# Kernel optimization log

Measured on AMD Instinct MI355X. Metric: run time of the kernel, lower is better.

## Reference

```python
import jax, jax.numpy as jnp
import numpy as np

N = 50000
E = 800000
IN_FEAT = 256
HIDDEN = 256
NUM_CLASS = 10
NUM_GRAPHS = 512
LAYERS = 2


def setup_inputs() -> dict:
    key = jax.random.key(0)
    ks = jax.random.split(key, 10)
    x = jax.random.normal(ks[0], (N, IN_FEAT), dtype=jnp.float32)
    edge_index = jax.random.randint(ks[1], (2, E), 0, N, dtype=jnp.int32)
    batch = jnp.sort(jax.random.randint(ks[2], (N,), 0, NUM_GRAPHS, dtype=jnp.int32))
    s_in = 1.0 / np.sqrt(IN_FEAT)
    s_h = 1.0 / np.sqrt(HIDDEN)
    enc_W = jax.random.uniform(ks[3], (IN_FEAT, HIDDEN), jnp.float32, -s_in, s_in)
    enc_b = jax.random.uniform(ks[4], (HIDDEN,), jnp.float32, -s_in, s_in)
    conv_W = jax.random.uniform(ks[5], (LAYERS, HIDDEN, HIDDEN), jnp.float32, -s_h, s_h)
    conv_b = jax.random.uniform(ks[6], (LAYERS, HIDDEN), jnp.float32, -s_h, s_h)
    out_W = jax.random.uniform(ks[7], (HIDDEN, NUM_CLASS), jnp.float32, -s_h, s_h)
    out_b = jax.random.uniform(ks[8], (NUM_CLASS,), jnp.float32, -s_h, s_h)
    return {"x": x, "edge_index": edge_index, "batch": batch,
            "enc_W": enc_W, "enc_b": enc_b,
            "conv_W": conv_W, "conv_b": conv_b,
            "out_W": out_W, "out_b": out_b}


def _gcn_conv(x, row, col, deg_norm_edge, W, b):
    # PyG GCNConv: linear transform, then normalized scatter-add aggregation.
    h = x @ W                                   # [N, H]
    msg = h[row] * deg_norm_edge[:, None]       # [E+N, H] gather + scale
    out = jax.ops.segment_sum(msg, col, num_segments=N)  # scatter-add
    return out + b


def reference(x, edge_index, batch, enc_W, enc_b, conv_W, conv_b, out_W, out_b):
    # self-loops appended once (same structure every layer)
    loops = jnp.arange(N, dtype=edge_index.dtype)
    row = jnp.concatenate([edge_index[0], loops])  # source
    col = jnp.concatenate([edge_index[1], loops])  # target
    deg = jax.ops.segment_sum(jnp.ones_like(col, dtype=x.dtype), col, num_segments=N)
    dinv = jnp.where(deg > 0, jax.lax.rsqrt(deg), 0.0)
    norm = dinv[row] * dinv[col]                # symmetric GCN normalization per edge

    h = x @ enc_W + enc_b
    for i in range(LAYERS):
        h = jax.nn.relu(_gcn_conv(h, row, col, norm, conv_W[i], conv_b[i]))

    # global_mean_pool over `batch` segment ids
    sums = jax.ops.segment_sum(h, batch, num_segments=NUM_GRAPHS)
    cnts = jax.ops.segment_sum(jnp.ones((N,), dtype=h.dtype), batch, num_segments=NUM_GRAPHS)
    pooled = sums / jnp.maximum(cnts, 1.0)[:, None]

    # dropout is identity in eval mode
    return pooled @ out_W + out_b
```

## Files before the change

kernel.cpp:

```cpp
#include <hip/hip_runtime.h>

#define NN 50000
#define NE 800000
#define HD 256
#define NG 512
#define NC 10
#define GEMM_G ((NN + 31) / 32)
#define NP 196
#define HB 200
#define CHUNK (NE / HB)
#define NODES_PER_HB (NN / HB)

typedef unsigned short u16;
typedef unsigned char u8;
typedef short v8s __attribute__((ext_vector_type(8)));
typedef float v4f __attribute__((ext_vector_type(4)));
typedef float v2f __attribute__((ext_vector_type(2)));
typedef u16 v4u __attribute__((ext_vector_type(4)));

static __device__ __forceinline__ float bf2f(u16 u) {
    return __uint_as_float(((unsigned)u) << 16);
}
static __device__ __forceinline__ u16 f2bf(float f) {
    unsigned u = __float_as_uint(f);
    unsigned r = (u + 0x7fffu + ((u >> 16) & 1u)) >> 16;
    return (u16)r;
}
static __device__ __forceinline__ int clampi(int v, int lo, int hi) {
    return min(max(v, lo), hi);
}
static __device__ __forceinline__ float ldf(const void* p, size_t i, int isbf) {
    return isbf ? bf2f(((const u16*)p)[i]) : ((const float*)p)[i];
}

static __device__ __forceinline__ u8 f32_to_fp8(float f) {
#if __has_builtin(__builtin_amdgcn_cvt_pk_fp8_f32)
    int r = __builtin_amdgcn_cvt_pk_fp8_f32(f, f, 0, false);
    return (u8)(r & 0xff);
#else
    float a = fabsf(f);
    unsigned s = (__float_as_uint(f) >> 31) << 7;
    if (a < 0.0009765625f) return (u8)s;
    a = fminf(a, 448.f);
    if (a < 0.015625f) {
        int m = (int)(a * 512.f + 0.5f);
        return (u8)(s | min(m, 7));
    }
    unsigned u = __float_as_uint(a);
    unsigned r = u + 0x0007FFFFu + ((u >> 20) & 1u);
    int e = (int)(r >> 23) - 127 + 7;
    if (e > 15) return (u8)(s | 0x7E);
    unsigned m = (r >> 20) & 7u;
    return (u8)(s | ((unsigned)e << 3) | m);
#endif
}
static __device__ __forceinline__ v4f fp8x4_to_f32(unsigned v) {
#if __has_builtin(__builtin_amdgcn_cvt_pk_f32_fp8)
    v2f lo = __builtin_amdgcn_cvt_pk_f32_fp8(v, false);
    v2f hi = __builtin_amdgcn_cvt_pk_f32_fp8(v, true);
    return (v4f){lo[0], lo[1], hi[0], hi[1]};
#else
    v4f o;
#pragma unroll
    for (int j = 0; j < 4; j++) {
        unsigned b = (v >> (8 * j)) & 0xffu;
        unsigned e = (b >> 3) & 15u, m = b & 7u;
        float val = e ? __uint_as_float(((e + 120u) << 23) | (m << 20))
                      : (float)m * 0.001953125f;
        o[j] = (b & 0x80u) ? -val : val;
    }
    return o;
#endif
}

__global__ void k_detect(const u16* __restrict__ xu, int* __restrict__ mode) {
    __shared__ int cnt;
    if (threadIdx.x == 0) cnt = 0;
    __syncthreads();
    int bad = 0;
    for (int i = threadIdx.x; i < 4096; i += 256) {
        float v = bf2f(xu[2 * i]);
        float av = fabsf(v);
        if (av > 100.f || (av < 1e-3f && av != 0.f)) bad++;
    }
    atomicAdd(&cnt, bad);
    __syncthreads();
    if (threadIdx.x == 0) mode[0] = (cnt > 1024) ? 0 : 1;
}

__global__ void k_prep(const void* __restrict__ enc_W, const void* __restrict__ conv_W,
                       const void* __restrict__ enc_b, const void* __restrict__ conv_b,
                       const void* __restrict__ out_b,
                       u16* __restrict__ Wp, float* __restrict__ biasf,
                       const int* __restrict__ modep) {
    int md = modep[0];
    int b = blockIdx.x;
    if (b < 768) {
        int wi = b >> 8;
        int n = b & 255, k = threadIdx.x;
        const void* W = (wi == 0) ? enc_W : conv_W;
        size_t off = (wi == 0) ? 0 : (size_t)(wi - 1) * HD * HD;
        int nt = n >> 4, m = n & 15;
        int ks = k >> 5, q = (k >> 3) & 3, j = k & 7;
        size_t idx = ((((size_t)nt * 8 + ks) * 64) + q * 16 + m) * 8 + j;
        Wp[(size_t)wi * HD * HD + idx] = f2bf(ldf(W, off + (size_t)k * HD + n, md));
    } else {
        for (int j = threadIdx.x; j < 768 + NC; j += 256) {
            float v = (j < 256) ? ldf(enc_b, j, md)
                    : (j < 768) ? ldf(conv_b, j - 256, md)
                                : ldf(out_b, j - 768, md);
            biasf[j] = v;
        }
    }
}

static __device__ __forceinline__ void hist_body(
        int b, const int* __restrict__ ecol, const int* __restrict__ batch,
        int* __restrict__ bh, int* __restrict__ gptr, int* hist) {
    int tid = threadIdx.x;
    if (tid < NP) hist[tid] = 0;
    __syncthreads();
    int e0 = b * CHUNK;
    for (int i = tid; i < CHUNK; i += 256) {
        int c = clampi(ecol[e0 + i], 0, NN - 1);
        atomicAdd(&hist[c >> 8], 1);
    }
    int n0 = b * NODES_PER_HB;
    for (int i = tid; i < NODES_PER_HB; i += 256) {
        int idx = n0 + i;
        int bb = clampi(batch[idx], 0, NG - 1);
        int bp = (idx == 0) ? -1 : clampi(batch[idx - 1], 0, NG - 1);
        for (int g = bp + 1; g <= bb; g++) gptr[g] = idx;
        if (idx == NN - 1)
            for (int g = bb + 1; g <= NG; g++) gptr[g] = NN;
    }
    __syncthreads();
    if (tid < NP) bh[(size_t)tid * HB + b] = hist[tid];
}

static __device__ __forceinline__ void scat_body(
        int b, const int* __restrict__ erow, const int* __restrict__ ecol,
        const int* __restrict__ pptr, const int* __restrict__ base,
        unsigned* __restrict__ pairbuf, int* lfill) {
    int tid = threadIdx.x;
    if (tid < NP) lfill[tid] = 0;
    __syncthreads();
    int e0 = b * CHUNK;
    for (int i = tid; i < CHUNK; i += 256) {
        int c = clampi(ecol[e0 + i], 0, NN - 1);
        int rw = clampi(erow[e0 + i], 0, NN - 1);
        int p = c >> 8;
        int r = atomicAdd(&lfill[p], 1);
        int pos = pptr[p] + base[(size_t)p * HB + b] + r;
        pairbuf[pos] = ((unsigned)rw << 8) | (unsigned)(c & 255);
    }
}

static __device__ __forceinline__ void gemm_body(
        int bid, u16* As, const void* __restrict__ A, const u16* __restrict__ Wp,
        const float* __restrict__ biasf, void* __restrict__ out,
        int M, int hasBias, int outFp8, int amode) {
    int tid = threadIdx.x;
    int wave = tid >> 6;
    int lane = tid & 63;
    int row0 = bid * 32;
    if (row0 >= M) return;
    int m = lane & 15, q = lane >> 4;

#pragma unroll
    for (int it = 0; it < 4; it++) {
        int fb = it * 4 + wave;
        int mt = fb >> 3, ks = fb & 7;
        int row = min(row0 + mt * 16 + m, M - 1);
        int colE = ks * 32 + q * 8;
        v8s v;
        if (amode) {
            v = *(const v8s*)((const u16*)A + (size_t)row * HD + colE);
        } else {
            const float* af = (const float*)A + (size_t)row * HD + colE;
            v4f x0 = *(const v4f*)af;
            v4f x1 = *(const v4f*)(af + 4);
            v[0] = (short)f2bf(x0[0]); v[1] = (short)f2bf(x0[1]);
            v[2] = (short)f2bf(x0[2]); v[3] = (short)f2bf(x0[3]);
            v[4] = (short)f2bf(x1[0]); v[5] = (short)f2bf(x1[1]);
            v[6] = (short)f2bf(x1[2]); v[7] = (short)f2bf(x1[3]);
        }
        *(v8s*)&As[((size_t)fb * 64 + lane) * 8] = v;
    }
    __syncthreads();

    v4f acc[2][4];
#pragma unroll
    for (int i = 0; i < 2; i++)
#pragma unroll
        for (int j = 0; j < 4; j++) acc[i][j] = (v4f){0.f, 0.f, 0.f, 0.f};

    const u16* wp = Wp + (size_t)wave * 4 * 8 * 64 * 8;

#pragma unroll
    for (int ks = 0; ks < 8; ks++) {
        v8s bfr[4];
#pragma unroll
        for (int nt = 0; nt < 4; nt++)
            bfr[nt] = *(const v8s*)(wp + ((size_t)(nt * 8 + ks) * 64 + lane) * 8);
        v8s a[2];
#pragma unroll
        for (int mt = 0; mt < 2; mt++)
            a[mt] = *(const v8s*)&As[((size_t)(mt * 8 + ks) * 64 + lane) * 8];
#pragma unroll
        for (int mt = 0; mt < 2; mt++)
#pragma unroll
            for (int nt = 0; nt < 4; nt++)
                acc[mt][nt] = __builtin_amdgcn_mfma_f32_16x16x32_bf16(
                    a[mt], bfr[nt], acc[mt][nt], 0, 0, 0);
    }
    if (outFp8) {
#pragma unroll
        for (int mt = 0; mt < 2; mt++) {
#pragma unroll
            for (int nt = 0; nt < 4; nt++) {
                int ocol = wave * 64 + nt * 16 + m;
#pragma unroll
                for (int r = 0; r < 4; r++) {
                    int orow = row0 + mt * 16 + q * 4 + r;
                    if (orow < M)
                        ((u8*)out)[(size_t)orow * HD + ocol] =
                            f32_to_fp8(acc[mt][nt][r] * 32.f);
                }
            }
        }
    } else {
#pragma unroll
        for (int mt = 0; mt < 2; mt++) {
#pragma unroll
            for (int nt = 0; nt < 4; nt++) {
                int ocol = wave * 64 + nt * 16 + m;
                float badd = hasBias ? biasf[ocol] : 0.f;
#pragma unroll
                for (int r = 0; r < 4; r++) {
                    int orow = row0 + mt * 16 + q * 4 + r;
                    if (orow < M)
                        ((u16*)out)[(size_t)orow * HD + ocol] =
                            f2bf(acc[mt][nt][r] + badd);
                }
            }
        }
    }
}

__global__ __launch_bounds__(256) void k_gemm(
        const void* __restrict__ A, const u16* __restrict__ Wp,
        const float* __restrict__ biasf, void* __restrict__ out,
        int M, int hasBias, int outFp8,
        const int* __restrict__ modep, int forceBf) {
    __shared__ u16 As[16 * 64 * 8];
    gemm_body(blockIdx.x, As, A, Wp, biasf, out, M, hasBias, outFp8,
              forceBf ? 1 : modep[0]);
}

__global__ __launch_bounds__(256) void k_hist(
        const int* __restrict__ ecol, const int* __restrict__ batch,
        int* __restrict__ bh, int* __restrict__ gptr) {
    __shared__ int hist[NP];
    hist_body(blockIdx.x, ecol, batch, bh, gptr, hist);
}

__global__ __launch_bounds__(256) void k_scat(
        const int* __restrict__ erow, const int* __restrict__ ecol,
        const int* __restrict__ pptr, const int* __restrict__ base,
        unsigned* __restrict__ pairbuf) {
    __shared__ int lfill[NP];
    scat_body(blockIdx.x, erow, ecol, pptr, base, pairbuf, lfill);
}

__global__ __launch_bounds__(256) void k_gemm_hist(
        const void* __restrict__ A, const u16* __restrict__ Wp,
        const float* __restrict__ biasf, void* __restrict__ out,
        int M, int hasBias, const int* __restrict__ modep, int forceBf,
        const int* __restrict__ ecol, const int* __restrict__ batch,
        int* __restrict__ bh, int* __restrict__ gptr) {
    __shared__ u16 As[16 * 64 * 8];
    __shared__ int hist[NP];
    if (blockIdx.x < HB) {
        hist_body(blockIdx.x, ecol, batch, bh, gptr, hist);
    } else {
        gemm_body(blockIdx.x - HB, As, A, Wp, biasf, out, M, hasBias, 0,
                  forceBf ? 1 : modep[0]);
    }
}

__global__ __launch_bounds__(256) void k_scat_gemm1(
        const void* __restrict__ A, const u16* __restrict__ Wp,
        void* __restrict__ out, int M,
        const int* __restrict__ erow, const int* __restrict__ ecol,
        const int* __restrict__ pptr, const int* __restrict__ base,
        unsigned* __restrict__ pairbuf) {
    __shared__ u16 As[16 * 64 * 8];
    __shared__ int lfill[NP];
    if (blockIdx.x < HB) {
        scat_body(blockIdx.x, erow, ecol, pptr, base, pairbuf, lfill);
    } else {
        gemm_body(blockIdx.x - HB, As, A, Wp, nullptr, out, M, 0, 1, 1);
    }
}

__global__ __launch_bounds__(256) void k_scanA(
        const int* __restrict__ bh, int* __restrict__ base, int* __restrict__ ptot) {
    int p = blockIdx.x, t = threadIdx.x;
    int v = (t < HB) ? bh[(size_t)p * HB + t] : 0;
    __shared__ int sh[256];
    sh[t] = v;
    __syncthreads();
    for (int off = 1; off < 256; off <<= 1) {
        int x = (t >= off) ? sh[t - off] : 0;
        __syncthreads();
        sh[t] += x;
        __syncthreads();
    }
    if (t < HB) base[(size_t)p * HB + t] = sh[t] - v;
    if (t == 0) ptot[p] = sh[255];
}

__global__ __launch_bounds__(256) void k_scanB(
        const int* __restrict__ ptot, int* __restrict__ pptr) {
    int t = threadIdx.x;
    int v = (t < NP) ? ptot[t] : 0;
    __shared__ int sh[256];
    sh[t] = v;
    __syncthreads();
    for (int off = 1; off < 256; off <<= 1) {
        int x = (t >= off) ? sh[t - off] : 0;
        __syncthreads();
        sh[t] += x;
        __syncthreads();
    }
    if (t < NP) pptr[t] = sh[t] - v;
    if (t == 0) pptr[NP] = sh[255];
}

__global__ __launch_bounds__(256) void k_part2(
        const int* __restrict__ pptr, const unsigned* __restrict__ pairbuf,
        int* __restrict__ cptr, float* __restrict__ dinv, int* __restrict__ csrc) {
    int p = blockIdx.x, t = threadIdx.x;
    int seg0 = pptr[p], seg1 = pptr[p + 1];
    __shared__ int hist[256], sums[256], fill[256];
    hist[t] = 0;
    fill[t] = 0;
    __syncthreads();
    for (int i = seg0 + t; i < seg1; i += 256)
        atomicAdd(&hist[pairbuf[i] & 255], 1);
    __syncthreads();
    int d = hist[t];
    sums[t] = d;
    __syncthreads();
    for (int off = 1; off < 256; off <<= 1) {
        int x = (t >= off) ? sums[t - off] : 0;
        __syncthreads();
        sums[t] += x;
        __syncthreads();
    }
    int ex = sums[t] - d;
    int c = p * 256 + t;
    if (c < NN) {
        cptr[c] = seg0 + ex;
        dinv[c] = rsqrtf((float)(d + 1));
    }
    if (p == NP - 1 && t == 0) cptr[NN] = NE;
    __syncthreads();
    sums[t] = ex;
    __syncthreads();
    for (int i = seg0 + t; i < seg1; i += 256) {
        unsigned v = pairbuf[i];
        int cl = v & 255;
        int r = atomicAdd(&fill[cl], 1);
        csrc[seg0 + sums[cl] + r] = (int)(v >> 8);
    }
}

__global__ __launch_bounds__(256) void k_aggregate(
        const u8* __restrict__ t, const int* __restrict__ cptr,
        const int* __restrict__ csrc, const float* __restrict__ dinv,
        const float* __restrict__ biasf, u16* __restrict__ out) {
    int wave = threadIdx.x >> 6;
    int lane = threadIdx.x & 63;
    int node = blockIdx.x * 4 + wave;
    if (node >= NN) return;
    int f0 = lane * 4;
    const u8* tf = t + f0;
    float dn = dinv[node];

    unsigned sv = *(const unsigned*)(tf + (size_t)node * HD);
    v4f sd = fp8x4_to_f32(sv);
    float a0 = sd[0] * dn, a1 = sd[1] * dn, a2 = sd[2] * dn, a3 = sd[3] * dn;

    int e0 = cptr[node], e1 = cptr[node + 1];
    e1 = clampi(e1, 0, NE);
    e0 = clampi(e0, 0, e1);
    int e = e0;
    for (; e + 8 <= e1; e += 8) {
        int s[8];
#pragma unroll
        for (int j = 0; j < 8; j++) s[j] = clampi(csrc[e + j], 0, NN - 1);
        unsigned rv[8];
        float wv[8];
#pragma unroll
        for (int j = 0; j < 8; j++) {
            rv[j] = *(const unsigned*)(tf + (size_t)s[j] * HD);
            wv[j] = dinv[s[j]];
        }
#pragma unroll
        for (int j = 0; j < 8; j++) {
            v4f d = fp8x4_to_f32(rv[j]);
            a0 = fmaf(d[0], wv[j], a0); a1 = fmaf(d[1], wv[j], a1);
            a2 = fmaf(d[2], wv[j], a2); a3 = fmaf(d[3], wv[j], a3);
        }
    }
    for (; e < e1; e++) {
        int src = clampi(csrc[e], 0, NN - 1);
        unsigned rv = *(const unsigned*)(tf + (size_t)src * HD);
        float wv = dinv[src];
        v4f d = fp8x4_to_f32(rv);
        a0 = fmaf(d[0], wv, a0); a1 = fmaf(d[1], wv, a1);
        a2 = fmaf(d[2], wv, a2); a3 = fmaf(d[3], wv, a3);
    }
    float sc = dn * 0.03125f;
    v4f b = *(const v4f*)(biasf + f0);
    a0 = fmaxf(a0 * sc + b[0], 0.f);
    a1 = fmaxf(a1 * sc + b[1], 0.f);
    a2 = fmaxf(a2 * sc + b[2], 0.f);
    a3 = fmaxf(a3 * sc + b[3], 0.f);
    v4u o = {f2bf(a0), f2bf(a1), f2bf(a2), f2bf(a3)};
    *(v4u*)(out + (size_t)node * HD + f0) = o;
}

__global__ __launch_bounds__(256) void k_head(
        const u16* __restrict__ h, const int* __restrict__ gptr,
        const void* __restrict__ W, const float* __restrict__ biasf,
        void* __restrict__ outv, const int* __restrict__ modep) {
    int md = modep[0];
    int g = blockIdx.x, f = threadIdx.x;
    int hi = clampi(gptr[g + 1], 0, NN);
    int lo = clampi(gptr[g], 0, hi);
    float s0 = 0.f, s1 = 0.f, s2 = 0.f, s3 = 0.f;
    int i = lo;
    for (; i + 4 <= hi; i += 4) {
        s0 += bf2f(h[(size_t)i * HD + f]);
        s1 += bf2f(h[(size_t)(i + 1) * HD + f]);
        s2 += bf2f(h[(size_t)(i + 2) * HD + f]);
        s3 += bf2f(h[(size_t)(i + 3) * HD + f]);
    }
    for (; i < hi; i++) s0 += bf2f(h[(size_t)i * HD + f]);
    __shared__ float ps[256];
    ps[f] = ((s0 + s1) + (s2 + s3)) / fmaxf((float)(hi - lo), 1.0f);
    __syncthreads();
    if (threadIdx.x < 64) {
        int lane = threadIdx.x;
        float acc[NC];
#pragma unroll
        for (int c = 0; c < NC; c++) acc[c] = 0.f;
        for (int k = lane; k < HD; k += 64) {
            float p = ps[k];
#pragma unroll
            for (int c = 0; c < NC; c++) acc[c] += p * ldf(W, (size_t)k * NC + c, md);
        }
#pragma unroll
        for (int c = 0; c < NC; c++) {
            for (int off = 32; off > 0; off >>= 1)
                acc[c] += __shfl_down(acc[c], off, 64);
        }
        if (lane == 0) {
#pragma unroll
            for (int c = 0; c < NC; c++) {
                float vv = acc[c] + biasf[768 + c];
                if (md) ((u16*)outv)[g * NC + c] = f2bf(vv);
                else    ((float*)outv)[g * NC + c] = vv;
            }
        }
    }
}

extern "C" void kernel_launch(void* const* d_in, const int* in_sizes, int n_in,
                              void* d_out, int out_size, void* d_ws, size_t ws_size,
                              hipStream_t stream) {
    const void* x      = d_in[0];
    const int*  ei     = (const int*)d_in[1];
    const int*  batch  = (const int*)d_in[2];
    const void* enc_W  = d_in[3];
    const void* enc_b  = d_in[4];
    const void* conv_W = d_in[5];
    const void* conv_b = d_in[6];
    const void* out_W  = d_in[7];
    const void* out_b  = d_in[8];

    char* w = (char*)d_ws;
    auto alloc = [&](size_t b) { char* p = w; w += (b + 255) & ~(size_t)255; return p; };
    int*   mode   = (int*)alloc(256);
    float* dinv   = (float*)alloc(NN * 4);
    int*   cptr   = (int*)alloc((NN + 1) * 4);
    int*   gptr   = (int*)alloc((NG + 1) * 4);
    int*   csrc   = (int*)alloc((size_t)NE * 4);
    u16*   Wp     = (u16*)alloc((size_t)3 * HD * HD * 2);
    float* biasf  = (float*)alloc(778 * 4);
    u16*   hbuf   = (u16*)alloc((size_t)NN * HD * 2);
    size_t scratch_need = ((size_t)2 * NP * HB + 2 * NP + 1) * 4 + (size_t)NE * 4 + 1024;
    size_t used = (size_t)(w - (char*)d_ws);
    bool fused = (used + scratch_need <= ws_size);
    char* sb = fused ? alloc(scratch_need) : (char*)hbuf;
    int* bh   = (int*)sb;
    int* base = bh + (size_t)NP * HB;
    int* ptot = base + (size_t)NP * HB;
    int* pptr = ptot + NP;
    unsigned* pairbuf = (unsigned*)(pptr + NP + 1);
    u8* tbuf = (u8*)d_in[0];

    const int* erow = ei;
    const int* ecol = ei + NE;

    k_detect<<<1, 256, 0, stream>>>((const u16*)x, mode);
    k_prep<<<769, 256, 0, stream>>>(enc_W, conv_W, enc_b, conv_b, out_b, Wp, biasf, mode);

    if (fused) {
        k_gemm_hist<<<HB + GEMM_G, 256, 0, stream>>>(
            x, Wp, biasf, hbuf, NN, 1, mode, 0, ecol, batch, bh, gptr);
        k_scanA<<<NP, 256, 0, stream>>>(bh, base, ptot);
        k_scanB<<<1, 256, 0, stream>>>(ptot, pptr);
        k_scat_gemm1<<<HB + GEMM_G, 256, 0, stream>>>(
            hbuf, Wp + (size_t)HD * HD, tbuf, NN, erow, ecol, pptr, base, pairbuf);
        k_part2<<<NP, 256, 0, stream>>>(pptr, pairbuf, cptr, dinv, csrc);
    } else {
        k_hist<<<HB, 256, 0, stream>>>(ecol, batch, bh, gptr);
        k_scanA<<<NP, 256, 0, stream>>>(bh, base, ptot);
        k_scanB<<<1, 256, 0, stream>>>(ptot, pptr);
        k_scat<<<HB, 256, 0, stream>>>(erow, ecol, pptr, base, pairbuf);
        k_part2<<<NP, 256, 0, stream>>>(pptr, pairbuf, cptr, dinv, csrc);
        k_gemm<<<GEMM_G, 256, 0, stream>>>(x, Wp, biasf, hbuf, NN, 1, 0, mode, 0);
        k_gemm<<<GEMM_G, 256, 0, stream>>>(hbuf, Wp + (size_t)HD * HD, nullptr,
                                           tbuf, NN, 0, 1, mode, 1);
    }
    k_aggregate<<<(NN + 3) / 4, 256, 0, stream>>>(tbuf, cptr, csrc, dinv,
                                                  biasf + 256, hbuf);
    k_gemm<<<GEMM_G, 256, 0, stream>>>(hbuf, Wp + (size_t)2 * HD * HD, nullptr,
                                       tbuf, NN, 0, 1, mode, 1);
    k_aggregate<<<(NN + 3) / 4, 256, 0, stream>>>(tbuf, cptr, csrc, dinv,
                                                  biasf + 256 + HD, hbuf);
    k_head<<<NG, 256, 0, stream>>>(hbuf, gptr, out_W, biasf, d_out, mode);
}
```

Baseline: 285.0 us.

## Fuse layer-1 aggregation with layer-2 GEMM and widen aggregate lanes

Adds a fused kernel that gathers and aggregates the layer-1 neighbour messages for 32 nodes into shared memory as bf16, then multiplies the tile by the next conv weight with MFMA and writes fp8 output to a new buffer. This removes one bf16 round trip of the hidden activations and one kernel launch. The aggregation is also rewritten so each lane handles 8 features and the two half-waves split the edges, combined with a cross-half shuffle, giving wider loads and more memory parallelism. The fused path needs an extra N*HD workspace buffer, and the fused kernel runs gather work with fewer waves per node tile, which could lower latency hiding.

```diff
diff --git a/kernel.cpp b/kernel.cpp
--- a/kernel.cpp
+++ b/kernel.cpp
@@ -17,6 +17,7 @@
 typedef float v4f __attribute__((ext_vector_type(4)));
 typedef float v2f __attribute__((ext_vector_type(2)));
 typedef u16 v4u __attribute__((ext_vector_type(4)));
+typedef u16 v8u __attribute__((ext_vector_type(8)));
 
 static __device__ __forceinline__ float bf2f(u16 u) {
     return __uint_as_float(((unsigned)u) << 16);
@@ -248,6 +249,89 @@
     }
 }
 
+static __device__ __forceinline__ void agg_node(
+        const u8* __restrict__ t, const int* __restrict__ cptr,
+        const int* __restrict__ csrc, const float* __restrict__ dinv,
+        const float* __restrict__ biasf, int node, int lane, float* o) {
+    int half = lane >> 5;
+    int f0 = (lane & 31) * 8;
+    const u8* tf = t + f0;
+    float dn = dinv[node];
+    float a[8];
+#pragma unroll
+    for (int k = 0; k < 8; k++) a[k] = 0.f;
+
+    if (half == 0) {
+        uint2 sv = *(const uint2*)(tf + (size_t)node * HD);
+        v4f lo = fp8x4_to_f32(sv.x), hi = fp8x4_to_f32(sv.y);
+#pragma unroll
+        for (int k = 0; k < 4; k++) {
+            a[k] += lo[k] * dn;
+            a[k + 4] += hi[k] * dn;
+        }
+    }
+
+    int e0 = cptr[node], e1 = cptr[node + 1];
+    e1 = clampi(e1, 0, NE);
+    e0 = clampi(e0, 0, e1);
+    int e = e0;
+    for (; e + 16 <= e1; e += 16) {
+        int s[8];
+#pragma unroll
+        for (int j = 0; j < 8; j++)
+            s[j] = clampi(csrc[e + 2 * j + half], 0, NN - 1);
+        uint2 rv[8];
+        float wv[8];
+#pragma unroll
+        for (int j = 0; j < 8; j++) {
+            rv[j] = *(const uint2*)(tf + (size_t)s[j] * HD);
+            wv[j] = dinv[s[j]];
+        }
+#pragma unroll
+        for (int j = 0; j < 8; j++) {
+            v4f lo = fp8x4_to_f32(rv[j].x), hi = fp8x4_to_f32(rv[j].y);
+#pragma unroll
+            for (int k = 0; k < 4; k++) {
+                a[k] = fmaf(lo[k], wv[j], a[k]);
+                a[k + 4] = fmaf(hi[k], wv[j], a[k + 4]);
+            }
+        }
+    }
+    for (; e + 2 <= e1; e += 2) {
+        int s = clampi(csrc[e + half], 0, NN - 1);
+        uint2 rv = *(const uint2*)(tf + (size_t)s * HD);
+        float wv = dinv[s];
+        v4f lo = fp8x4_to_f32(rv.x), hi = fp8x4_to_f32(rv.y);
+#pragma unroll
+        for (int k = 0; k < 4; k++) {
+            a[k] = fmaf(lo[k], wv, a[k]);
+            a[k + 4] = fmaf(hi[k], wv, a[k + 4]);
+        }
+    }
+    if (e < e1 && half == 0) {
+        int s = clampi(csrc[e], 0, NN - 1);
+        uint2 rv = *(const uint2*)(tf + (size_t)s * HD);
+        float wv = dinv[s];
+        v4f lo = fp8x4_to_f32(rv.x), hi = fp8x4_to_f32(rv.y);
+#pragma unroll
+        for (int k = 0; k < 4; k++) {
+            a[k] = fmaf(lo[k], wv, a[k]);
+            a[k + 4] = fmaf(hi[k], wv, a[k + 4]);
+        }
+    }
+#pragma unroll
+    for (int k = 0; k < 8; k++) a[k] += __shfl_xor(a[k], 32, 64);
+
+    float sc = dn * 0.03125f;
+    v4f b0 = *(const v4f*)(biasf + f0);
+    v4f b1 = *(const v4f*)(biasf + f0 + 4);
+#pragma unroll
+    for (int k = 0; k < 4; k++) {
+        o[k] = fmaxf(fmaf(a[k], sc, b0[k]), 0.f);
+        o[k + 4] = fmaxf(fmaf(a[k + 4], sc, b1[k]), 0.f);
+    }
+}
+
 __global__ __launch_bounds__(256) void k_gemm(
         const void* __restrict__ A, const u16* __restrict__ Wp,
         const float* __restrict__ biasf, void* __restrict__ out,
@@ -304,6 +388,89 @@
     }
 }
 
+__global__ __launch_bounds__(256) void k_agg_gemm(
+        const u8* __restrict__ t, const int* __restrict__ cptr,
+        const int* __restrict__ csrc, const float* __restrict__ dinv,
+        const float* __restrict__ biasf, const u16* __restrict__ Wp2,
+        u8* __restrict__ out) {
+    __shared__ u16 As2[32 * 264];
+    int tid = threadIdx.x, wave = tid >> 6, lane = tid & 63;
+    int row0 = blockIdx.x * 32;
+
+    for (int it = 0; it < 8; it++) {
+        int r = wave * 8 + it;
+        int node = row0 + r;
+        float o[8];
+#pragma unroll
+        for (int k = 0; k < 8; k++) o[k] = 0.f;
+        if (node < NN) agg_node(t, cptr, csrc, dinv, biasf, node, lane, o);
+        if (lane < 32) {
+            v8u pk;
+#pragma unroll
+            for (int k = 0; k < 8; k++) pk[k] = f2bf(o[k]);
+            *(v8u*)&As2[r * 264 + lane * 8] = pk;
+        }
+    }
+    __syncthreads();
+
+    int m = lane & 15, q = lane >> 4;
+    v4f acc[2][4];
+#pragma unroll
+    for (int i = 0; i < 2; i++)
+#pragma unroll
+        for (int j = 0; j < 4; j++) acc[i][j] = (v4f){0.f, 0.f, 0.f, 0.f};
+
+    const u16* wp = Wp2 + (size_t)wave * 4 * 8 * 64 * 8;
+#pragma unroll
+    for (int ks = 0; ks < 8; ks++) {
+        v8s bfr[4];
+#pragma unroll
+        for (int nt = 0; nt < 4; nt++)
+            bfr[nt] = *(const v8s*)(wp + ((size_t)(nt * 8 + ks) * 64 + lane) * 8);
+        v8s a[2];
+#pragma unroll
+        for (int mt = 0; mt < 2; mt++)
+            a[mt] = *(const v8s*)&As2[(mt * 16 + m) * 264 + ks * 32 + q * 8];
+#pragma unroll
+        for (int mt = 0; mt < 2; mt++)
+#pragma unroll
+            for (int nt = 0; nt < 4; nt++)
+                acc[mt][nt] = __builtin_amdgcn_mfma_f32_16x16x32_bf16(
+                    a[mt], bfr[nt], acc[mt][nt], 0, 0, 0);
+    }
+#pragma unroll
+    for (int mt = 0; mt < 2; mt++) {
+#pragma unroll
+        for (int nt = 0; nt < 4; nt++) {
+            int ocol = wave * 64 + nt * 16 + m;
+#pragma unroll
+            for (int r = 0; r < 4; r++) {
+                int orow = row0 + mt * 16 + q * 4 + r;
+                if (orow < NN)
+                    out[(size_t)orow * HD + ocol] =
+                        f32_to_fp8(acc[mt][nt][r] * 32.f);
+            }
+        }
+    }
+}
+
+__global__ __launch_bounds__(256) void k_aggregate2(
+        const u8* __restrict__ t, const int* __restrict__ cptr,
+        const int* __restrict__ csrc, const float* __restrict__ dinv,
+        const float* __restrict__ biasf, u16* __restrict__ out) {
+    int wave = threadIdx.x >> 6, lane = threadIdx.x & 63;
+    int node = blockIdx.x * 4 + wave;
+    if (node >= NN) return;
+    float o[8];
+    agg_node(t, cptr, csrc, dinv, biasf, node, lane, o);
+    if (lane < 32) {
+        v8u pk;
+#pragma unroll
+        for (int k = 0; k < 8; k++) pk[k] = f2bf(o[k]);
+        *(v8u*)(out + (size_t)node * HD + lane * 8) = pk;
+    }
+}
+
 __global__ __launch_bounds__(256) void k_scanA(
         const int* __restrict__ bh, int* __restrict__ base, int* __restrict__ ptot) {
     int p = blockIdx.x, t = threadIdx.x;
@@ -375,62 +542,6 @@
         int r = atomicAdd(&fill[cl], 1);
         csrc[seg0 + sums[cl] + r] = (int)(v >> 8);
     }
-}
-
-__global__ __launch_bounds__(256) void k_aggregate(
-        const u8* __restrict__ t, const int* __restrict__ cptr,
-        const int* __restrict__ csrc, const float* __restrict__ dinv,
-        const float* __restrict__ biasf, u16* __restrict__ out) {
-    int wave = threadIdx.x >> 6;
-    int lane = threadIdx.x & 63;
-    int node = blockIdx.x * 4 + wave;
-    if (node >= NN) return;
-    int f0 = lane * 4;
-    const u8* tf = t + f0;
-    float dn = dinv[node];
-
-    unsigned sv = *(const unsigned*)(tf + (size_t)node * HD);
-    v4f sd = fp8x4_to_f32(sv);
-    float a0 = sd[0] * dn, a1 = sd[1] * dn, a2 = sd[2] * dn, a3 = sd[3] * dn;
-
-    int e0 = cptr[node], e1 = cptr[node + 1];
-    e1 = clampi(e1, 0, NE);
-    e0 = clampi(e0, 0, e1);
-    int e = e0;
-    for (; e + 8 <= e1; e += 8) {
-        int s[8];
-#pragma unroll
-        for (int j = 0; j < 8; j++) s[j] = clampi(csrc[e + j], 0, NN - 1);
-        unsigned rv[8];
-        float wv[8];
-#pragma unroll
-        for (int j = 0; j < 8; j++) {
-            rv[j] = *(const unsigned*)(tf + (size_t)s[j] * HD);
-            wv[j] = dinv[s[j]];
-        }
-#pragma unroll
-        for (int j = 0; j < 8; j++) {
-            v4f d = fp8x4_to_f32(rv[j]);
-            a0 = fmaf(d[0], wv[j], a0); a1 = fmaf(d[1], wv[j], a1);
-            a2 = fmaf(d[2], wv[j], a2); a3 = fmaf(d[3], wv[j], a3);
-        }
-    }
-    for (; e < e1; e++) {
-        int src = clampi(csrc[e], 0, NN - 1);
-        unsigned rv = *(const unsigned*)(tf + (size_t)src * HD);
-        float wv = dinv[src];
-        v4f d = fp8x4_to_f32(rv);
-        a0 = fmaf(d[0], wv, a0); a1 = fmaf(d[1], wv, a1);
-        a2 = fmaf(d[2], wv, a2); a3 = fmaf(d[3], wv, a3);
-    }
-    float sc = dn * 0.03125f;
-    v4f b = *(const v4f*)(biasf + f0);
-    a0 = fmaxf(a0 * sc + b[0], 0.f);
-    a1 = fmaxf(a1 * sc + b[1], 0.f);
-    a2 = fmaxf(a2 * sc + b[2], 0.f);
-    a3 = fmaxf(a3 * sc + b[3], 0.f);
-    v4u o = {f2bf(a0), f2bf(a1), f2bf(a2), f2bf(a3)};
-    *(v4u*)(out + (size_t)node * HD + f0) = o;
 }
 
 __global__ __launch_bounds__(256) void k_head(
@@ -503,9 +614,11 @@
     float* biasf  = (float*)alloc(778 * 4);
     u16*   hbuf   = (u16*)alloc((size_t)NN * HD * 2);
     size_t scratch_need = ((size_t)2 * NP * HB + 2 * NP + 1) * 4 + (size_t)NE * 4 + 1024;
+    size_t tbuf2_need = (size_t)NN * HD;
     size_t used = (size_t)(w - (char*)d_ws);
-    bool fused = (used + scratch_need <= ws_size);
+    bool fused = (used + scratch_need + tbuf2_need + 512 <= ws_size);
     char* sb = fused ? alloc(scratch_need) : (char*)hbuf;
+    u8* tbuf2 = fused ? (u8*)alloc(tbuf2_need) : nullptr;
     int* bh   = (int*)sb;
     int* base = bh + (size_t)NP * HB;
     int* ptot = base + (size_t)NP * HB;
@@ -527,6 +640,10 @@
         k_scat_gemm1<<<HB + GEMM_G, 256, 0, stream>>>(
             hbuf, Wp + (size_t)HD * HD, tbuf, NN, erow, ecol, pptr, base, pairbuf);
         k_part2<<<NP, 256, 0, stream>>>(pptr, pairbuf, cptr, dinv, csrc);
+        k_agg_gemm<<<GEMM_G, 256, 0, stream>>>(
+            tbuf, cptr, csrc, dinv, biasf + 256, Wp + (size_t)2 * HD * HD, tbuf2);
+        k_aggregate2<<<(NN + 3) / 4, 256, 0, stream>>>(
+            tbuf2, cptr, csrc, dinv, biasf + 256 + HD, hbuf);
     } else {
         k_hist<<<HB, 256, 0, stream>>>(ecol, batch, bh, gptr);
         k_scanA<<<NP, 256, 0, stream>>>(bh, base, ptot);
@@ -536,12 +653,12 @@
         k_gemm<<<GEMM_G, 256, 0, stream>>>(x, Wp, biasf, hbuf, NN, 1, 0, mode, 0);
         k_gemm<<<GEMM_G, 256, 0, stream>>>(hbuf, Wp + (size_t)HD * HD, nullptr,
                                            tbuf, NN, 0, 1, mode, 1);
-    }
-    k_aggregate<<<(NN + 3) / 4, 256, 0, stream>>>(tbuf, cptr, csrc, dinv,
-                                                  biasf + 256, hbuf);
-    k_gemm<<<GEMM_G, 256, 0, stream>>>(hbuf, Wp + (size_t)2 * HD * HD, nullptr,
-                                       tbuf, NN, 0, 1, mode, 1);
-    k_aggregate<<<(NN + 3) / 4, 256, 0, stream>>>(tbuf, cptr, csrc, dinv,
-                                                  biasf + 256 + HD, hbuf);
+        k_aggregate2<<<(NN + 3) / 4, 256, 0, stream>>>(
+            tbuf, cptr, csrc, dinv, biasf + 256, hbuf);
+        k_gemm<<<GEMM_G, 256, 0, stream>>>(hbuf, Wp + (size_t)2 * HD * HD, nullptr,
+                                           tbuf, NN, 0, 1, mode, 1);
+        k_aggregate2<<<(NN + 3) / 4, 256, 0, stream>>>(
+            tbuf, cptr, csrc, dinv, biasf + 256 + HD, hbuf);
+    }
     k_head<<<NG, 256, 0, stream>>>(hbuf, gptr, out_W, biasf, d_out, mode);
 }
```

Result: slower. 330.7 us (+16.0%).

## Store fp8 transform output in feature slabs and aggregate per slab

Applied to the files above, without the earlier changes.

The GEMM's fp8 output is now written in four 64-feature slabs (slab-major, then node), so each slab of the message table is 3.2 MB instead of 12.8 MB and fits better in cache. The aggregation kernel launches four times as many blocks, one per slab and node group. Within a wave, four sub-groups of 16 lanes handle different edges in parallel and are combined with cross-lane shuffles. The aim is better cache locality for the random gathers and more edge-level parallelism. The cost is that CSR indices and dinv are read once per slab, and a shuffle reduction is added.

```diff
diff --git a/kernel.cpp b/kernel.cpp
--- a/kernel.cpp
+++ b/kernel.cpp
@@ -10,6 +10,7 @@
 #define HB 200
 #define CHUNK (NE / HB)
 #define NODES_PER_HB (NN / HB)
+#define NB ((NN + 3) / 4)
 
 typedef unsigned short u16;
 typedef unsigned char u8;
@@ -224,8 +225,8 @@
                 for (int r = 0; r < 4; r++) {
                     int orow = row0 + mt * 16 + q * 4 + r;
                     if (orow < M)
-                        ((u8*)out)[(size_t)orow * HD + ocol] =
-                            f32_to_fp8(acc[mt][nt][r] * 32.f);
+                        ((u8*)out)[((size_t)(ocol >> 6) * NN + orow) * 64 +
+                                   (ocol & 63)] = f32_to_fp8(acc[mt][nt][r] * 32.f);
                 }
             }
         }
@@ -304,6 +305,77 @@
     }
 }
 
+__global__ __launch_bounds__(256) void k_agg_slab(
+        const u8* __restrict__ t, const int* __restrict__ cptr,
+        const int* __restrict__ csrc, const float* __restrict__ dinv,
+        const float* __restrict__ biasf, u16* __restrict__ out) {
+    int sl = blockIdx.x / NB, nb = blockIdx.x % NB;
+    int wave = threadIdx.x >> 6, lane = threadIdx.x & 63;
+    int node = nb * 4 + wave;
+    if (node >= NN) return;
+    int sub = lane >> 4;
+    int fb = (lane & 15) * 4;
+    const u8* ts = t + (size_t)sl * NN * 64 + fb;
+    float dn = dinv[node];
+    float a0 = 0.f, a1 = 0.f, a2 = 0.f, a3 = 0.f;
+
+    if (sub == 0) {
+        unsigned sv = *(const unsigned*)(ts + (size_t)node * 64);
+        v4f d = fp8x4_to_f32(sv);
+        a0 = d[0] * dn; a1 = d[1] * dn; a2 = d[2] * dn; a3 = d[3] * dn;
+    }
+
+    int e0 = cptr[node], e1 = cptr[node + 1];
+    e1 = clampi(e1, 0, NE);
+    e0 = clampi(e0, 0, e1);
+    int e = e0;
+    for (; e + 16 <= e1; e += 16) {
+        int s4[4];
+#pragma unroll
+        for (int j = 0; j < 4; j++)
+            s4[j] = clampi(csrc[e + 4 * j + sub], 0, NN - 1);
+        unsigned rv[4];
+        float wv[4];
+#pragma unroll
+        for (int j = 0; j < 4; j++) {
+            rv[j] = *(const unsigned*)(ts + (size_t)s4[j] * 64);
+            wv[j] = dinv[s4[j]];
+        }
+#pragma unroll
+        for (int j = 0; j < 4; j++) {
+            v4f d = fp8x4_to_f32(rv[j]);
+            a0 = fmaf(d[0], wv[j], a0); a1 = fmaf(d[1], wv[j], a1);
+            a2 = fmaf(d[2], wv[j], a2); a3 = fmaf(d[3], wv[j], a3);
+        }
+    }
+    for (; e < e1; e += 4) {
+        int idx = e + sub;
+        bool vld = idx < e1;
+        int sv = vld ? clampi(csrc[idx], 0, NN - 1) : node;
+        unsigned rv = *(const unsigned*)(ts + (size_t)sv * 64);
+        float wv = vld ? dinv[sv] : 0.f;
+        v4f d = fp8x4_to_f32(rv);
+        a0 = fmaf(d[0], wv, a0); a1 = fmaf(d[1], wv, a1);
+        a2 = fmaf(d[2], wv, a2); a3 = fmaf(d[3], wv, a3);
+    }
+
+    a0 += __shfl_xor(a0, 16, 64); a0 += __shfl_xor(a0, 32, 64);
+    a1 += __shfl_xor(a1, 16, 64); a1 += __shfl_xor(a1, 32, 64);
+    a2 += __shfl_xor(a2, 16, 64); a2 += __shfl_xor(a2, 32, 64);
+    a3 += __shfl_xor(a3, 16, 64); a3 += __shfl_xor(a3, 32, 64);
+
+    if (sub == 0) {
+        float sc = dn * 0.03125f;
+        v4f b = *(const v4f*)(biasf + sl * 64 + (lane & 15) * 4);
+        v4u pk;
+        pk[0] = f2bf(fmaxf(fmaf(a0, sc, b[0]), 0.f));
+        pk[1] = f2bf(fmaxf(fmaf(a1, sc, b[1]), 0.f));
+        pk[2] = f2bf(fmaxf(fmaf(a2, sc, b[2]), 0.f));
+        pk[3] = f2bf(fmaxf(fmaf(a3, sc, b[3]), 0.f));
+        *(v4u*)(out + (size_t)node * HD + sl * 64 + (lane & 15) * 4) = pk;
+    }
+}
+
 __global__ __launch_bounds__(256) void k_scanA(
         const int* __restrict__ bh, int* __restrict__ base, int* __restrict__ ptot) {
     int p = blockIdx.x, t = threadIdx.x;
@@ -375,62 +447,6 @@
         int r = atomicAdd(&fill[cl], 1);
         csrc[seg0 + sums[cl] + r] = (int)(v >> 8);
     }
-}
-
-__global__ __launch_bounds__(256) void k_aggregate(
-        const u8* __restrict__ t, const int* __restrict__ cptr,
-        const int* __restrict__ csrc, const float* __restrict__ dinv,
-        const float* __restrict__ biasf, u16* __restrict__ out) {
-    int wave = threadIdx.x >> 6;
-    int lane = threadIdx.x & 63;
-    int node = blockIdx.x * 4 + wave;
-    if (node >= NN) return;
-    int f0 = lane * 4;
-    const u8* tf = t + f0;
-    float dn = dinv[node];
-
-    unsigned sv = *(const unsigned*)(tf + (size_t)node * HD);
-    v4f sd = fp8x4_to_f32(sv);
-    float a0 = sd[0] * dn, a1 = sd[1] * dn, a2 = sd[2] * dn, a3 = sd[3] * dn;
-
-    int e0 = cptr[node], e1 = cptr[node + 1];
-    e1 = clampi(e1, 0, NE);
-    e0 = clampi(e0, 0, e1);
-    int e = e0;
-    for (; e + 8 <= e1; e += 8) {
-        int s[8];
-#pragma unroll
-        for (int j = 0; j < 8; j++) s[j] = clampi(csrc[e + j], 0, NN - 1);
-        unsigned rv[8];
-        float wv[8];
-#pragma unroll
-        for (int j = 0; j < 8; j++) {
-            rv[j] = *(const unsigned*)(tf + (size_t)s[j] * HD);
-            wv[j] = dinv[s[j]];
-        }
-#pragma unroll
-        for (int j = 0; j < 8; j++) {
-            v4f d = fp8x4_to_f32(rv[j]);
-            a0 = fmaf(d[0], wv[j], a0); a1 = fmaf(d[1], wv[j], a1);
-            a2 = fmaf(d[2], wv[j], a2); a3 = fmaf(d[3], wv[j], a3);
-        }
-    }
-    for (; e < e1; e++) {
-        int src = clampi(csrc[e], 0, NN - 1);
-        unsigned rv = *(const unsigned*)(tf + (size_t)src * HD);
-        float wv = dinv[src];
-        v4f d = fp8x4_to_f32(rv);
-        a0 = fmaf(d[0], wv, a0); a1 = fmaf(d[1], wv, a1);
-        a2 = fmaf(d[2], wv, a2); a3 = fmaf(d[3], wv, a3);
-    }
-    float sc = dn * 0.03125f;
-    v4f b = *(const v4f*)(biasf + f0);
-    a0 = fmaxf(a0 * sc + b[0], 0.f);
-    a1 = fmaxf(a1 * sc + b[1], 0.f);
-    a2 = fmaxf(a2 * sc + b[2], 0.f);
-    a3 = fmaxf(a3 * sc + b[3], 0.f);
-    v4u o = {f2bf(a0), f2bf(a1), f2bf(a2), f2bf(a3)};
-    *(v4u*)(out + (size_t)node * HD + f0) = o;
 }
 
 __global__ __launch_bounds__(256) void k_head(
@@ -537,11 +553,11 @@
         k_gemm<<<GEMM_G, 256, 0, stream>>>(hbuf, Wp + (size_t)HD * HD, nullptr,
                                            tbuf, NN, 0, 1, mode, 1);
     }
-    k_aggregate<<<(NN + 3) / 4, 256, 0, stream>>>(tbuf, cptr, csrc, dinv,
-                                                  biasf + 256, hbuf);
+    k_agg_slab<<<4 * NB, 256, 0, stream>>>(tbuf, cptr, csrc, dinv,
+                                           biasf + 256, hbuf);
     k_gemm<<<GEMM_G, 256, 0, stream>>>(hbuf, Wp + (size_t)2 * HD * HD, nullptr,
                                        tbuf, NN, 0, 1, mode, 1);
-    k_aggregate<<<(NN + 3) / 4, 256, 0, stream>>>(tbuf, cptr, csrc, dinv,
-                                                  biasf + 256 + HD, hbuf);
+    k_agg_slab<<<4 * NB, 256, 0, stream>>>(tbuf, cptr, csrc, dinv,
+                                           biasf + 256 + HD, hbuf);
     k_head<<<NG, 256, 0, stream>>>(hbuf, gptr, out_W, biasf, d_out, mode);
 }
```

New measurement: 383.0 us. 34.4% more time.
